# Kernel optimization log

Measured on AMD Instinct MI355X. Metric: run time of the kernel, lower is better.

The kernel has to match this reference:

```python
import jax, jax.numpy as jnp
import numpy as np

N_NODES = 100000
N_EDGES = 1600000
D = 128
N_GRAPHS = 8


def setup_inputs() -> dict:
    key = jax.random.key(0)
    ks = jax.random.split(key, 10)
    x = jax.random.normal(ks[0], (N_NODES, D), dtype=jnp.float32)
    src = jax.random.randint(ks[1], (N_EDGES,), 0, N_NODES)
    dst = jax.random.randint(ks[2], (N_EDGES,), 0, N_NODES)
    graph_ids = jnp.sort(jax.random.randint(ks[3], (N_NODES,), 0, N_GRAPHS))
    s = 1.0 / np.sqrt(D)
    W1 = jax.random.normal(ks[4], (D, D), dtype=jnp.float32) * s
    b1 = jnp.zeros((D,), dtype=jnp.float32)
    W2 = jax.random.normal(ks[5], (D, D), dtype=jnp.float32) * s
    b2 = jnp.zeros((D,), dtype=jnp.float32)
    prelu_a = jnp.full((1,), 0.25, dtype=jnp.float32)
    lin_W = jax.random.normal(ks[6], (D, 1), dtype=jnp.float32) * s
    lin_b = jnp.zeros((1,), dtype=jnp.float32)
    return {"x": x, "src": src, "dst": dst, "graph_ids": graph_ids,
            "W1": W1, "b1": b1, "W2": W2, "b2": b2,
            "prelu_a": prelu_a, "lin_W": lin_W, "lin_b": lin_b}


def _gcn_layer(h, src, dst, n_src, n_dst, W, b):
    # GraphConv with symmetric ('both') normalization: D^{-1/2} A D^{-1/2} H W + b
    h = h @ W                                      # [N, D] small GEMM
    m = h[src] * n_src[:, None]                    # [E, D] gather (irregular)
    agg = jax.ops.segment_sum(m, dst, num_segments=N_NODES)  # scatter-add
    return agg * n_dst[:, None] + b


def reference(x, src, dst, graph_ids, W1, b1, W2, b2, prelu_a, lin_W, lin_b):
    ones_e = jnp.ones((src.shape[0],), dtype=x.dtype)
    deg_out = jnp.maximum(jax.ops.segment_sum(ones_e, src, num_segments=N_NODES), 1.0)
    deg_in = jnp.maximum(jax.ops.segment_sum(ones_e, dst, num_segments=N_NODES), 1.0)
    n_src = jax.lax.rsqrt(deg_out)[src]            # per-edge source norm
    n_dst = jax.lax.rsqrt(deg_in)                  # per-node dest norm

    h = _gcn_layer(x, src, dst, n_src, n_dst, W1, b1)
    h = jax.nn.relu(h)
    h = _gcn_layer(h, src, dst, n_src, n_dst, W2, b2)
    h = jax.nn.relu(h)

    # dgl.mean_nodes: per-graph mean over nodes
    sums = jax.ops.segment_sum(h, graph_ids, num_segments=N_GRAPHS)   # [G, D]
    cnt = jax.ops.segment_sum(jnp.ones((N_NODES,), h.dtype), graph_ids,
                              num_segments=N_GRAPHS)
    pooled = sums / jnp.maximum(cnt, 1.0)[:, None]

    # PReLU (single shared slope) -> Linear -> Sigmoid
    pooled = jnp.where(pooled > 0, pooled, prelu_a[0] * pooled)
    out = jax.nn.sigmoid(pooled @ lin_W + lin_b)   # [G, 1]
    return out
```

## Files before the change

kernel.cpp:

```cpp
#include <hip/hip_runtime.h>
#include <hip/hip_bf16.h>

#define NN 100000
#define NE 1600000
#define DD 128
#define NG 8

#define BSH 8
#define KB 391
#define BMASK 255
#define PB 512
#define CHUNK 3125
#define SCAN_N (KB * PB)
#define GHB 98

typedef unsigned short u16;
typedef unsigned char u8;
typedef __attribute__((ext_vector_type(8))) short short8;
typedef __attribute__((ext_vector_type(4))) float f32x4;
typedef __attribute__((ext_vector_type(2))) float f32x2;

static __device__ __forceinline__ u16 f2bf(float f) {
  unsigned u = __float_as_uint(f);
  u += 0x7fffu + ((u >> 16) & 1);
  return (u16)(u >> 16);
}
static __device__ __forceinline__ u8 f2fp8(float f) {
  return (u8)(__builtin_amdgcn_cvt_pk_fp8_f32(f, f, 0, false) & 0xFF);
}

__global__ __launch_bounds__(256) void p1x(const int* __restrict__ src,
                                           const int* __restrict__ dst,
                                           int* __restrict__ countsS,
                                           int* __restrict__ countsD,
                                           const float* __restrict__ W1,
                                           const float* __restrict__ W2,
                                           u16* __restrict__ Wt1,
                                           u16* __restrict__ Wt2,
                                           const int* __restrict__ gid,
                                           int* __restrict__ cnt_part,
                                           float* __restrict__ pooled) {
  __shared__ int hs[KB], hd[KB];
  __shared__ int h8[NG];
  int t = threadIdx.x, b = blockIdx.x;
  if (b < PB) {
    for (int i = t; i < KB; i += 256) { hs[i] = 0; hd[i] = 0; }
    __syncthreads();
    int e0 = b * CHUNK;
    for (int i = t; i < CHUNK; i += 256) {
      atomicAdd(&hs[src[e0 + i] >> BSH], 1);
      atomicAdd(&hd[dst[e0 + i] >> BSH], 1);
    }
    __syncthreads();
    for (int i = t; i < KB; i += 256) {
      countsS[i * PB + b] = hs[i];
      countsD[i * PB + b] = hd[i];
    }
  } else if (b < PB + 128) {
    int i = (b - PB) * 256 + t;
    if (i < DD * DD) {
      int n = i >> 7, k = i & 127;
      Wt1[i] = f2bf(W1[k * DD + n]);
    } else {
      int i2 = i - DD * DD;
      int n = i2 >> 7, k = i2 & 127;
      Wt2[i2] = f2bf(W2[k * DD + n]);
    }
  } else if (b < PB + 128 + GHB) {
    int blk = b - PB - 128;
    if (t < NG) h8[t] = 0;
    __syncthreads();
    for (int i = blk * 256 + t; i < NN; i += GHB * 256)
      atomicAdd(&h8[gid[i]], 1);
    __syncthreads();
    if (t < NG) cnt_part[blk * NG + t] = h8[t];
  } else {
    for (int i = t; i < NG * DD; i += 256) pooled[i] = 0.f;
  }
}

__global__ __launch_bounds__(256) void scanA(int* __restrict__ countsS,
                                             int* __restrict__ countsD,
                                             int* __restrict__ totS,
                                             int* __restrict__ totD) {
  __shared__ int data[PB];
  __shared__ int part[256];
  int b = blockIdx.x;
  int isS = (b < KB);
  int k = isS ? b : b - KB;
  int* counts = isS ? countsS : countsD;
  int* tot = isS ? totS : totD;
  int t = threadIdx.x;
  int* c = counts + (size_t)k * PB;
  data[t] = c[t];
  data[t + 256] = c[t + 256];
  __syncthreads();
  int a0 = data[2 * t], a1 = data[2 * t + 1];
  int s = a0 + a1;
  part[t] = s;
  __syncthreads();
  for (int off = 1; off < 256; off <<= 1) {
    int v = (t >= off) ? part[t - off] : 0;
    __syncthreads();
    part[t] += v;
    __syncthreads();
  }
  int ex = part[t] - s;
  data[2 * t] = ex;
  data[2 * t + 1] = ex + a0;
  __syncthreads();
  c[t] = data[t];
  c[t + 256] = data[t + 256];
  if (t == 255) tot[k] = part[255];
}

static __device__ __forceinline__ void exscan512(int t, int* data, int* part,
                                                 int* out, int nmax) {
  __syncthreads();
  int a0 = data[2 * t], a1 = data[2 * t + 1];
  int s = a0 + a1;
  part[t] = s;
  __syncthreads();
  for (int off = 1; off < 256; off <<= 1) {
    int v = (t >= off) ? part[t - off] : 0;
    __syncthreads();
    part[t] += v;
    __syncthreads();
  }
  int ex = part[t] - s;
  if (2 * t <= nmax) out[2 * t] = ex;
  if (2 * t + 1 <= nmax) out[2 * t + 1] = ex + a0;
  __syncthreads();
}

__global__ __launch_bounds__(256) void p2x(const int* __restrict__ src,
                                           const int* __restrict__ dst,
                                           const int* __restrict__ countsS,
                                           const int* __restrict__ countsD,
                                           const int* __restrict__ totS,
                                           const int* __restrict__ totD,
                                           int* __restrict__ baseS,
                                           int* __restrict__ baseD,
                                           u8* __restrict__ recsS,
                                           unsigned* __restrict__ recsD) {
  __shared__ int data[512];
  __shared__ int part[256];
  __shared__ int bS[KB + 1], bD[KB + 1];
  __shared__ int gS[KB], gD[KB];
  __shared__ int lsS[KB + 1], lsD[KB + 1];
  __shared__ int lcS[KB], lcD[KB];
  __shared__ unsigned stD[CHUNK];
  __shared__ u16 bkD[CHUNK];
  __shared__ u8 stS[CHUNK];
  __shared__ u16 bkS[CHUNK];
  int t = threadIdx.x, blk = blockIdx.x;

  data[t] = (t < KB) ? totS[t] : 0;
  data[t + 256] = (t + 256 < KB) ? totS[t + 256] : 0;
  exscan512(t, data, part, bS, KB);
  data[t] = (t < KB) ? totD[t] : 0;
  data[t + 256] = (t + 256 < KB) ? totD[t + 256] : 0;
  exscan512(t, data, part, bD, KB);

  if (blk == 0) {
    for (int i = t; i <= KB; i += 256) {
      baseS[i] = bS[i];
      baseD[i] = bD[i];
    }
  }

  for (int k = t; k < 512; k += 256) {
    int cnt = 0;
    if (k < KB) {
      int pref = countsS[k * PB + blk];
      int nxt = (blk < PB - 1) ? countsS[k * PB + blk + 1] : totS[k];
      cnt = nxt - pref;
      gS[k] = bS[k] + pref;
    }
    data[k] = cnt;
  }
  exscan512(t, data, part, lsS, KB);
  for (int k = t; k < 512; k += 256) {
    int cnt = 0;
    if (k < KB) {
      int pref = countsD[k * PB + blk];
      int nxt = (blk < PB - 1) ? countsD[k * PB + blk + 1] : totD[k];
      cnt = nxt - pref;
      gD[k] = bD[k] + pref;
    }
    data[k] = cnt;
  }
  exscan512(t, data, part, lsD, KB);

  for (int k = t; k < KB; k += 256) {
    lcS[k] = lsS[k];
    lcD[k] = lsD[k];
  }
  __syncthreads();

  int e0 = blk * CHUNK;
  for (int i = t; i < CHUNK; i += 256) {
    int s = src[e0 + i];
    int d = dst[e0 + i];
    int ks = s >> BSH;
    int kd = d >> BSH;
    int ps = atomicAdd(&lcS[ks], 1);
    stS[ps] = (u8)(s & BMASK);
    bkS[ps] = (u16)ks;
    int pd = atomicAdd(&lcD[kd], 1);
    stD[pd] = (unsigned)s | ((unsigned)(d & BMASK) << 17);
    bkD[pd] = (u16)kd;
  }
  __syncthreads();

  for (int i = t; i < CHUNK; i += 256) {
    int kd = bkD[i];
    recsD[gD[kd] + (i - lsD[kd])] = stD[i];
    int ks = bkS[i];
    recsS[gS[ks] + (i - lsS[ks])] = stS[i];
  }
}

__global__ __launch_bounds__(256) void sd_p3x(const u8* __restrict__ recsS,
                                              const int* __restrict__ baseS,
                                              float* __restrict__ rs_out,
                                              const float* __restrict__ x,
                                              u8* __restrict__ bufA,
                                              const unsigned* __restrict__ recsD,
                                              const int* __restrict__ baseD,
                                              int* __restrict__ csr_src,
                                              int* __restrict__ cursor_end,
                                              int* __restrict__ deg_in,
                                              float* __restrict__ rs_in) {
  __shared__ int hist[256];
  __shared__ int part[256];
  __shared__ float rsl[256];
  int t = threadIdx.x;
  if (blockIdx.x < KB) {
    int k = blockIdx.x;
    int rbeg = baseS[k];
    int rend = baseS[k + 1];
    hist[t] = 0;
    __syncthreads();
    for (int i = rbeg + t; i < rend; i += 256) atomicAdd(&hist[recsS[i]], 1);
    __syncthreads();
    int nbase = k << BSH;
    int n = nbase + t;
    float rv = rsqrtf(fmaxf((float)hist[t], 1.f));
    rsl[t] = rv;
    if (n < NN) rs_out[n] = rv;
    __syncthreads();
    for (int i = t; i < 256 * 16; i += 256) {
      int row = i >> 4, c = i & 15;
      int node = nbase + row;
      if (node >= NN) break;
      float w = rsl[row];
      const float4* p = (const float4*)(x + (size_t)node * DD + c * 8);
      float4 a = p[0], b = p[1];
      int lo = 0, hi = 0;
      lo = __builtin_amdgcn_cvt_pk_fp8_f32(a.x * w, a.y * w, lo, false);
      lo = __builtin_amdgcn_cvt_pk_fp8_f32(a.z * w, a.w * w, lo, true);
      hi = __builtin_amdgcn_cvt_pk_fp8_f32(b.x * w, b.y * w, hi, false);
      hi = __builtin_amdgcn_cvt_pk_fp8_f32(b.z * w, b.w * w, hi, true);
      *(uint2*)(bufA + (size_t)node * DD + c * 8) = make_uint2((unsigned)lo, (unsigned)hi);
    }
  } else {
    int k = blockIdx.x - KB;
    int rbeg = baseD[k];
    int rend = baseD[k + 1];
    hist[t] = 0;
    __syncthreads();
    for (int i = rbeg + t; i < rend; i += 256) atomicAdd(&hist[recsD[i] >> 17], 1);
    __syncthreads();
    int h = hist[t];
    part[t] = h;
    __syncthreads();
    for (int off = 1; off < 256; off <<= 1) {
      int v = (t >= off) ? part[t - off] : 0;
      __syncthreads();
      part[t] += v;
      __syncthreads();
    }
    int run = rbeg + part[t] - h;
    int n = (k << BSH) + t;
    if (n < NN) {
      cursor_end[n] = run + h;
      deg_in[n] = h;
      rs_in[n] = rsqrtf(fmaxf((float)h, 1.f));
    }
    hist[t] = run;
    __syncthreads();
    for (int i = rbeg + t; i < rend; i += 256) {
      unsigned r = recsD[i];
      int pos = atomicAdd(&hist[r >> 17], 1);
      csr_src[pos] = (int)(r & 0x1FFFF);
    }
  }
}

__global__ __launch_bounds__(256) void gather_agg_fp8(
    const uint4* __restrict__ Hv, const int* __restrict__ csr_src,
    const int* __restrict__ cursor_end, const int* __restrict__ deg_in,
    u16* __restrict__ agg) {
  int node = blockIdx.x * 32 + (threadIdx.x >> 3);
  if (node >= NN) return;
  int q = threadIdx.x & 7;
  int end = cursor_end[node];
  int j = end - deg_in[node];
  float acc[16];
#pragma unroll
  for (int i = 0; i < 16; ++i) acc[i] = 0.f;
#define ACCV(v) { f32x2 t_;                                                        \
  t_ = __builtin_amdgcn_cvt_pk_f32_fp8((int)(v).x, false); acc[0] += t_.x;  acc[1] += t_.y;  \
  t_ = __builtin_amdgcn_cvt_pk_f32_fp8((int)(v).x, true);  acc[2] += t_.x;  acc[3] += t_.y;  \
  t_ = __builtin_amdgcn_cvt_pk_f32_fp8((int)(v).y, false); acc[4] += t_.x;  acc[5] += t_.y;  \
  t_ = __builtin_amdgcn_cvt_pk_f32_fp8((int)(v).y, true);  acc[6] += t_.x;  acc[7] += t_.y;  \
  t_ = __builtin_amdgcn_cvt_pk_f32_fp8((int)(v).z, false); acc[8] += t_.x;  acc[9] += t_.y;  \
  t_ = __builtin_amdgcn_cvt_pk_f32_fp8((int)(v).z, true);  acc[10] += t_.x; acc[11] += t_.y; \
  t_ = __builtin_amdgcn_cvt_pk_f32_fp8((int)(v).w, false); acc[12] += t_.x; acc[13] += t_.y; \
  t_ = __builtin_amdgcn_cvt_pk_f32_fp8((int)(v).w, true);  acc[14] += t_.x; acc[15] += t_.y; }
  for (; j + 4 <= end; j += 4) {
    int s0 = csr_src[j + 0];
    int s1 = csr_src[j + 1];
    int s2 = csr_src[j + 2];
    int s3 = csr_src[j + 3];
    uint4 v0 = Hv[(size_t)s0 * 8 + q];
    uint4 v1 = Hv[(size_t)s1 * 8 + q];
    uint4 v2 = Hv[(size_t)s2 * 8 + q];
    uint4 v3 = Hv[(size_t)s3 * 8 + q];
    ACCV(v0) ACCV(v1) ACCV(v2) ACCV(v3)
  }
  for (; j < end; ++j) {
    uint4 v = Hv[(size_t)csr_src[j] * 8 + q];
    ACCV(v)
  }
#undef ACCV
  uint4 o0, o1;
  o0.x = (unsigned)f2bf(acc[0])  | ((unsigned)f2bf(acc[1])  << 16);
  o0.y = (unsigned)f2bf(acc[2])  | ((unsigned)f2bf(acc[3])  << 16);
  o0.z = (unsigned)f2bf(acc[4])  | ((unsigned)f2bf(acc[5])  << 16);
  o0.w = (unsigned)f2bf(acc[6])  | ((unsigned)f2bf(acc[7])  << 16);
  o1.x = (unsigned)f2bf(acc[8])  | ((unsigned)f2bf(acc[9])  << 16);
  o1.y = (unsigned)f2bf(acc[10]) | ((unsigned)f2bf(acc[11]) << 16);
  o1.z = (unsigned)f2bf(acc[12]) | ((unsigned)f2bf(acc[13]) << 16);
  o1.w = (unsigned)f2bf(acc[14]) | ((unsigned)f2bf(acc[15]) << 16);
  u16* op = agg + (size_t)node * DD + q * 16;
  *(uint4*)op = o0;
  *(uint4*)(op + 8) = o1;
}

#define GEMM_PRE                                                              \
  __shared__ uint4 Wl4[2048];                                      \
  int tid = threadIdx.x;                                                      \
  {                                                                           \
    const uint4* Wg4 = (const uint4*)Wt;                                      \
    for (int i = tid; i < 2048; i += 256) {                                   \
      int row = i >> 4, c = i & 15;                                           \
      Wl4[(row << 4) | (c ^ (row & 15))] = Wg4[i];                            \
    }                                                                         \
  }                                                                           \
  int wid = tid >> 6;                                                         \
  int lane = tid & 63;                                                        \
  int l15 = lane & 15;                                                        \
  int kg = lane >> 4;                                                         \
  int rowbase = blockIdx.x * 128 + wid * 32;                                  \
  f32x4 acc[2][8];                                                            \
  short8 a[2][4];                                                             \
  _Pragma("unroll")                                                           \
  for (int t = 0; t < 2; ++t) {                                               \
    int arow = rowbase + t * 16 + l15;                                        \
    bool ok = arow < NN;                                                      \
    const u16* aptr = Ab + (size_t)arow * DD + kg * 8;                        \
    _Pragma("unroll")                                                         \
    for (int kt = 0; kt < 4; ++kt) {                                          \
      a[t][kt] = ok ? *(const short8*)(aptr + kt * 32)                        \
                    : (short8){0, 0, 0, 0, 0, 0, 0, 0};                       \
      acc[0][kt] = (f32x4){0.f, 0.f, 0.f, 0.f};                               \
      acc[0][kt + 4] = (f32x4){0.f, 0.f, 0.f, 0.f};                           \
      acc[1][kt] = (f32x4){0.f, 0.f, 0.f, 0.f};                               \
      acc[1][kt + 4] = (f32x4){0.f, 0.f, 0.f, 0.f};                           \
    }                                                                         \
  }                                                                           \
  __syncthreads();                                                            \
  _Pragma("unroll")                                                           \
  for (int n = 0; n < 8; ++n) {                                               \
    _Pragma("unroll")                                                         \
    for (int kt = 0; kt < 4; ++kt) {                                          \
      short8 b = *(const short8*)(Wl4 + (((n * 16 + l15) << 4) |              \
                                         ((kg + kt * 4) ^ l15)));             \
      acc[0][n] = __builtin_amdgcn_mfma_f32_16x16x32_bf16(a[0][kt], b, acc[0][n], 0, 0, 0); \
      acc[1][n] = __builtin_amdgcn_mfma_f32_16x16x32_bf16(a[1][kt], b, acc[1][n], 0, 0, 0); \
    }                                                                         \
  }

__global__ __launch_bounds__(256) void gemm_mfma_fp8out(
    const u16* __restrict__ Ab, const u16* __restrict__ Wt,
    const float* __restrict__ bias, const float* __restrict__ rs,
    const float* __restrict__ post, u8* __restrict__ Cb) {
  GEMM_PRE
#pragma unroll
  for (int t = 0; t < 2; ++t) {
    int crow0 = rowbase + t * 16 + kg * 4;
#pragma unroll
    for (int j = 0; j < 4; ++j) {
      int r = crow0 + j;
      if (r < NN) {
        float s = rs[r];
        float ps = post[r];
#pragma unroll
        for (int n = 0; n < 8; ++n) {
          float v = fmaxf(acc[t][n][j] * s + bias[n * 16 + l15], 0.f) * ps;
          Cb[(size_t)r * DD + n * 16 + l15] = f2fp8(v);
        }
      }
    }
  }
}

__global__ __launch_bounds__(256) void gemm_mfma_pool(
    const u16* __restrict__ Ab, const u16* __restrict__ Wt,
    const float* __restrict__ bias, const float* __restrict__ rs,
    const int* __restrict__ gid, float* __restrict__ pooled) {
  __shared__ float pl[NG * DD];
  for (int i = threadIdx.x; i < NG * DD; i += 256) pl[i] = 0.f;
  GEMM_PRE
  float pacc[8];
#pragma unroll
  for (int n = 0; n < 8; ++n) pacc[n] = 0.f;
  int curg = -1;
#pragma unroll
  for (int t = 0; t < 2; ++t) {
    int crow0 = rowbase + t * 16 + kg * 4;
#pragma unroll
    for (int j = 0; j < 4; ++j) {
      int r = crow0 + j;
      if (r < NN) {
        int g = gid[r];
        if (g != curg) {
          if (curg >= 0) {
#pragma unroll
            for (int n = 0; n < 8; ++n) {
              atomicAdd(&pl[curg * DD + n * 16 + l15], pacc[n]);
              pacc[n] = 0.f;
            }
          }
          curg = g;
        }
        float s = rs[r];
#pragma unroll
        for (int n = 0; n < 8; ++n)
          pacc[n] += fmaxf(acc[t][n][j] * s + bias[n * 16 + l15], 0.f);
      }
    }
  }
  if (curg >= 0) {
#pragma unroll
    for (int n = 0; n < 8; ++n)
      atomicAdd(&pl[curg * DD + n * 16 + l15], pacc[n]);
  }
  __syncthreads();
  int rlo = blockIdx.x * 128;
  int rhi = rlo + 127;
  if (rhi >= NN) rhi = NN - 1;
  int gmin = gid[rlo];
  int gmax = gid[rhi];
  int span = (gmax - gmin + 1) * DD;
  for (int i = tid; i < span; i += 256) {
    float v = pl[gmin * DD + i];
    if (v != 0.f) atomicAdd(&pooled[gmin * DD + i], v);
  }
}

__global__ __launch_bounds__(128) void final_kernel(const float* __restrict__ pooled,
                                                    const int* __restrict__ cnt_part,
                                                    const float* __restrict__ prelu_a,
                                                    const float* __restrict__ linW,
                                                    const float* __restrict__ linb,
                                                    float* __restrict__ out) {
  int t = threadIdx.x;
  __shared__ float red[2];
  __shared__ int cntl[NG];
  if (t < NG) {
    int s = 0;
    for (int b = 0; b < GHB; ++b) s += cnt_part[b * NG + t];
    cntl[t] = s;
  }
  __syncthreads();
  float w = linW[t];
  float alpha = prelu_a[0];
  float lb = linb[0];
  for (int g = 0; g < NG; ++g) {
    float v = pooled[g * DD + t] / fmaxf((float)cntl[g], 1.f);
    v = v > 0.f ? v : alpha * v;
    float p = v * w;
#pragma unroll
    for (int off = 32; off >= 1; off >>= 1) p += __shfl_down(p, off, 64);
    if ((t & 63) == 0) red[t >> 6] = p;
    __syncthreads();
    if (t == 0) {
      float s = red[0] + red[1] + lb;
      out[g] = 1.f / (1.f + expf(-s));
    }
    __syncthreads();
  }
}

extern "C" void kernel_launch(void* const* d_in, const int* in_sizes, int n_in,
                              void* d_out, int out_size, void* d_ws, size_t ws_size,
                              hipStream_t stream) {
  const float* x   = (const float*)d_in[0];
  const int*   src = (const int*)d_in[1];
  const int*   dst = (const int*)d_in[2];
  const int*   gid = (const int*)d_in[3];
  const float* W1  = (const float*)d_in[4];
  const float* b1  = (const float*)d_in[5];
  const float* W2  = (const float*)d_in[6];
  const float* b2  = (const float*)d_in[7];
  const float* pa  = (const float*)d_in[8];
  const float* lW  = (const float*)d_in[9];
  const float* lb  = (const float*)d_in[10];
  float* out = (float*)d_out;

  char* ws = (char*)d_ws;
  size_t o = 0;
  auto alloc = [&](size_t bytes) {
    size_t r = o;
    o += (bytes + 255) & ~(size_t)255;
    return r;
  };
  int*   deg_in  = (int*)(ws + alloc((size_t)NN * 4));
  float* rs_out  = (float*)(ws + alloc((size_t)NN * 4));
  float* rs_in   = (float*)(ws + alloc((size_t)NN * 4));
  int*   countsS = (int*)(ws + alloc((size_t)SCAN_N * 4));
  int*   countsD = (int*)(ws + alloc((size_t)SCAN_N * 4));
  int*   totS    = (int*)(ws + alloc((size_t)KB * 4));
  int*   totD    = (int*)(ws + alloc((size_t)KB * 4));
  int*   baseS   = (int*)(ws + alloc((size_t)(KB + 1) * 4));
  int*   baseD   = (int*)(ws + alloc((size_t)(KB + 1) * 4));
  int*   cursor_end = (int*)(ws + alloc((size_t)NN * 4));
  u8*    recsS   = (u8*)(ws + alloc((size_t)NE));
  unsigned* recsD = (unsigned*)(ws + alloc((size_t)NE * 4));
  int*   csr_src = (int*)(ws + alloc((size_t)NE * 4));
  u16*   Wt1     = (u16*)(ws + alloc((size_t)DD * DD * 2));
  u16*   Wt2     = (u16*)(ws + alloc((size_t)DD * DD * 2));
  u8*    bufA    = (u8*)(ws + alloc((size_t)NN * DD));
  u8*    bufB    = (u8*)(ws + alloc((size_t)NN * DD));
  u16*   aggbuf  = (u16*)(ws + alloc((size_t)NN * DD * 2));
  float* pooled  = (float*)(ws + alloc((size_t)NG * DD * 4));
  int*   cnt_part = (int*)(ws + alloc((size_t)GHB * NG * 4));

  p1x<<<PB + 128 + GHB + 1, 256, 0, stream>>>(src, dst, countsS, countsD,
                                              W1, W2, Wt1, Wt2, gid, cnt_part, pooled);
  scanA<<<2 * KB, 256, 0, stream>>>(countsS, countsD, totS, totD);
  p2x<<<PB, 256, 0, stream>>>(src, dst, countsS, countsD, totS, totD,
                              baseS, baseD, recsS, recsD);
  sd_p3x<<<2 * KB, 256, 0, stream>>>(recsS, baseS, rs_out, x, bufA,
                                     recsD, baseD, csr_src, cursor_end, deg_in, rs_in);

  const int gablocks = (NN + 31) / 32;
  const int gmblocks = (NN + 127) / 128;

  gather_agg_fp8<<<gablocks, 256, 0, stream>>>((const uint4*)bufA, csr_src, cursor_end, deg_in, aggbuf);
  gemm_mfma_fp8out<<<gmblocks, 256, 0, stream>>>(aggbuf, Wt1, b1, rs_in, rs_out, bufB);
  gather_agg_fp8<<<gablocks, 256, 0, stream>>>((const uint4*)bufB, csr_src, cursor_end, deg_in, aggbuf);
  gemm_mfma_pool<<<gmblocks, 256, 0, stream>>>(aggbuf, Wt2, b2, rs_in, gid, pooled);
  final_kernel<<<1, 128, 0, stream>>>(pooled, cnt_part, pa, lW, lb, out);
}
```

Before: 174.2 us.

## Split fp8 feature matrix into four column slices for cache-local gathers

```diff
diff --git a/kernel.cpp b/kernel.cpp
--- a/kernel.cpp
+++ b/kernel.cpp
@@ -262,7 +262,10 @@
       lo = __builtin_amdgcn_cvt_pk_fp8_f32(a.z * w, a.w * w, lo, true);
       hi = __builtin_amdgcn_cvt_pk_fp8_f32(b.x * w, b.y * w, hi, false);
       hi = __builtin_amdgcn_cvt_pk_fp8_f32(b.z * w, b.w * w, hi, true);
-      *(uint2*)(bufA + (size_t)node * DD + c * 8) = make_uint2((unsigned)lo, (unsigned)hi);
+      int sl = c >> 2;
+      int off = (c & 3) * 8;
+      *(uint2*)(bufA + ((size_t)sl * NN + node) * 32 + off) =
+          make_uint2((unsigned)lo, (unsigned)hi);
     }
   } else {
     int k = blockIdx.x - KB;
@@ -298,55 +301,45 @@
   }
 }
 
-__global__ __launch_bounds__(256) void gather_agg_fp8(
-    const uint4* __restrict__ Hv, const int* __restrict__ csr_src,
+__global__ __launch_bounds__(256) void gather_slice4(
+    const u8* __restrict__ Hb, const int* __restrict__ csr_src,
     const int* __restrict__ cursor_end, const int* __restrict__ deg_in,
     u16* __restrict__ agg) {
-  int node = blockIdx.x * 32 + (threadIdx.x >> 3);
+  int sl = blockIdx.x & 3;
+  int node = (blockIdx.x >> 2) * 64 + (threadIdx.x >> 2);
   if (node >= NN) return;
-  int q = threadIdx.x & 7;
+  int ll = threadIdx.x & 3;
+  const uint2* H = (const uint2*)(Hb + (size_t)sl * NN * 32);
   int end = cursor_end[node];
   int j = end - deg_in[node];
-  float acc[16];
-#pragma unroll
-  for (int i = 0; i < 16; ++i) acc[i] = 0.f;
-#define ACCV(v) { f32x2 t_;                                                        \
-  t_ = __builtin_amdgcn_cvt_pk_f32_fp8((int)(v).x, false); acc[0] += t_.x;  acc[1] += t_.y;  \
-  t_ = __builtin_amdgcn_cvt_pk_f32_fp8((int)(v).x, true);  acc[2] += t_.x;  acc[3] += t_.y;  \
-  t_ = __builtin_amdgcn_cvt_pk_f32_fp8((int)(v).y, false); acc[4] += t_.x;  acc[5] += t_.y;  \
-  t_ = __builtin_amdgcn_cvt_pk_f32_fp8((int)(v).y, true);  acc[6] += t_.x;  acc[7] += t_.y;  \
-  t_ = __builtin_amdgcn_cvt_pk_f32_fp8((int)(v).z, false); acc[8] += t_.x;  acc[9] += t_.y;  \
-  t_ = __builtin_amdgcn_cvt_pk_f32_fp8((int)(v).z, true);  acc[10] += t_.x; acc[11] += t_.y; \
-  t_ = __builtin_amdgcn_cvt_pk_f32_fp8((int)(v).w, false); acc[12] += t_.x; acc[13] += t_.y; \
-  t_ = __builtin_amdgcn_cvt_pk_f32_fp8((int)(v).w, true);  acc[14] += t_.x; acc[15] += t_.y; }
+  float a0 = 0.f, a1 = 0.f, a2 = 0.f, a3 = 0.f, a4 = 0.f, a5 = 0.f, a6 = 0.f, a7 = 0.f;
+#define ACC2(v) { f32x2 t_;                                                  \
+  t_ = __builtin_amdgcn_cvt_pk_f32_fp8((int)(v).x, false); a0 += t_.x; a1 += t_.y; \
+  t_ = __builtin_amdgcn_cvt_pk_f32_fp8((int)(v).x, true);  a2 += t_.x; a3 += t_.y; \
+  t_ = __builtin_amdgcn_cvt_pk_f32_fp8((int)(v).y, false); a4 += t_.x; a5 += t_.y; \
+  t_ = __builtin_amdgcn_cvt_pk_f32_fp8((int)(v).y, true);  a6 += t_.x; a7 += t_.y; }
   for (; j + 4 <= end; j += 4) {
     int s0 = csr_src[j + 0];
     int s1 = csr_src[j + 1];
     int s2 = csr_src[j + 2];
     int s3 = csr_src[j + 3];
-    uint4 v0 = Hv[(size_t)s0 * 8 + q];
-    uint4 v1 = Hv[(size_t)s1 * 8 + q];
-    uint4 v2 = Hv[(size_t)s2 * 8 + q];
-    uint4 v3 = Hv[(size_t)s3 * 8 + q];
-    ACCV(v0) ACCV(v1) ACCV(v2) ACCV(v3)
+    uint2 v0 = H[s0 * 4 + ll];
+    uint2 v1 = H[s1 * 4 + ll];
+    uint2 v2 = H[s2 * 4 + ll];
+    uint2 v3 = H[s3 * 4 + ll];
+    ACC2(v0) ACC2(v1) ACC2(v2) ACC2(v3)
   }
   for (; j < end; ++j) {
-    uint4 v = Hv[(size_t)csr_src[j] * 8 + q];
-    ACCV(v)
-  }
-#undef ACCV
-  uint4 o0, o1;
-  o0.x = (unsigned)f2bf(acc[0])  | ((unsigned)f2bf(acc[1])  << 16);
-  o0.y = (unsigned)f2bf(acc[2])  | ((unsigned)f2bf(acc[3])  << 16);
-  o0.z = (unsigned)f2bf(acc[4])  | ((unsigned)f2bf(acc[5])  << 16);
-  o0.w = (unsigned)f2bf(acc[6])  | ((unsigned)f2bf(acc[7])  << 16);
-  o1.x = (unsigned)f2bf(acc[8])  | ((unsigned)f2bf(acc[9])  << 16);
-  o1.y = (unsigned)f2bf(acc[10]) | ((unsigned)f2bf(acc[11]) << 16);
-  o1.z = (unsigned)f2bf(acc[12]) | ((unsigned)f2bf(acc[13]) << 16);
-  o1.w = (unsigned)f2bf(acc[14]) | ((unsigned)f2bf(acc[15]) << 16);
-  u16* op = agg + (size_t)node * DD + q * 16;
-  *(uint4*)op = o0;
-  *(uint4*)(op + 8) = o1;
+    uint2 v = H[csr_src[j] * 4 + ll];
+    ACC2(v)
+  }
+#undef ACC2
+  uint4 o;
+  o.x = (unsigned)f2bf(a0) | ((unsigned)f2bf(a1) << 16);
+  o.y = (unsigned)f2bf(a2) | ((unsigned)f2bf(a3) << 16);
+  o.z = (unsigned)f2bf(a4) | ((unsigned)f2bf(a5) << 16);
+  o.w = (unsigned)f2bf(a6) | ((unsigned)f2bf(a7) << 16);
+  *(uint4*)(agg + (size_t)node * DD + sl * 32 + ll * 8) = o;
 }
 
 #define GEMM_PRE                                                              \
@@ -410,7 +403,7 @@
 #pragma unroll
         for (int n = 0; n < 8; ++n) {
           float v = fmaxf(acc[t][n][j] * s + bias[n * 16 + l15], 0.f) * ps;
-          Cb[(size_t)r * DD + n * 16 + l15] = f2fp8(v);
+          Cb[((size_t)(n >> 1) * NN + r) * 32 + (n & 1) * 16 + l15] = f2fp8(v);
         }
       }
     }
@@ -557,12 +550,12 @@
   sd_p3x<<<2 * KB, 256, 0, stream>>>(recsS, baseS, rs_out, x, bufA,
                                      recsD, baseD, csr_src, cursor_end, deg_in, rs_in);
 
-  const int gablocks = (NN + 31) / 32;
+  const int gablocks = ((NN + 63) / 64) * 4;
   const int gmblocks = (NN + 127) / 128;
 
-  gather_agg_fp8<<<gablocks, 256, 0, stream>>>((const uint4*)bufA, csr_src, cursor_end, deg_in, aggbuf);
+  gather_slice4<<<gablocks, 256, 0, stream>>>(bufA, csr_src, cursor_end, deg_in, aggbuf);
   gemm_mfma_fp8out<<<gmblocks, 256, 0, stream>>>(aggbuf, Wt1, b1, rs_in, rs_out, bufB);
-  gather_agg_fp8<<<gablocks, 256, 0, stream>>>((const uint4*)bufB, csr_src, cursor_end, deg_in, aggbuf);
+  gather_slice4<<<gablocks, 256, 0, stream>>>(bufB, csr_src, cursor_end, deg_in, aggbuf);
   gemm_mfma_pool<<<gmblocks, 256, 0, stream>>>(aggbuf, Wt2, b2, rs_in, gid, pooled);
   final_kernel<<<1, 128, 0, stream>>>(pooled, cnt_part, pa, lW, lb, out);
 }
```

Result: slower. 201.4 us (+15.6%).
